# Kernel optimization log

Hardware: AMD Instinct MI355X
Metric: run time of the kernel (lower is better)

## Reference

```python
import jax, jax.numpy as jnp
import numpy as np

B, N, M, NUM_CLASSES = 16, 2048, 2048, 40


def setup_inputs() -> dict:
    key = jax.random.key(0)
    k1, k2, k3, k4 = jax.random.split(key, 4)
    reg = jax.random.normal(k1, (B, N, 3), dtype=jnp.float32)
    point1 = jax.random.normal(k2, (B, M, 3), dtype=jnp.float32)
    # pred is expected to be log-probabilities (output of log_softmax)
    pred = jax.nn.log_softmax(jax.random.normal(k3, (B, NUM_CLASSES), dtype=jnp.float32), axis=-1)
    target = jax.random.randint(k4, (B,), 0, NUM_CLASSES, dtype=jnp.int64)
    return {"reg": reg, "point1": point1, "pred": pred, "target": target}


def _chamfer(x, y):
    # x: [B, N, 3], y: [B, M, 3]
    x2 = jnp.sum(x * x, axis=-1)                      # [B, N]
    y2 = jnp.sum(y * y, axis=-1)                      # [B, M]
    xy = jnp.einsum('bnd,bmd->bnm', x, y)             # [B, N, M]
    d = x2[:, :, None] + y2[:, None, :] - 2.0 * xy    # [B, N, M]
    dist1 = jnp.min(d, axis=2)                        # [B, N] nearest y for each x
    dist2 = jnp.min(d, axis=1)                        # [B, M] nearest x for each y
    return dist1, dist2


def reference(reg, point1, pred, target):
    # NLL loss with mean reduction: -mean(pred[b, target[b]])
    nll = -jnp.mean(jnp.take_along_axis(pred, target[:, None].astype(jnp.int32), axis=1))
    dist1, dist2 = _chamfer(reg, point1)
    reg_loss = jnp.mean(jnp.mean(dist1, axis=1) + jnp.mean(dist2, axis=1))
    return nll + reg_loss
```

## Files before the change

kernel.cpp:

```cpp
#include <hip/hip_runtime.h>
#include <hip/hip_bf16.h>


#define NPTS 2048
#define BATCH 16
#define NCLS 40
#define QB   128
#define KQ   8
#define NSEG 32
#define SEGLEN (NPTS / NSEG)
#define THREADS (QB / KQ * NSEG)

__global__ __launch_bounds__(64) void nll_init_kernel(const float* __restrict__ pred,
                                                      const int* __restrict__ target,
                                                      float* __restrict__ out) {
    int lane = threadIdx.x;
    float v = 0.f;
    if (lane < BATCH) v = pred[lane * NCLS + target[lane]];
    for (int off = 32; off > 0; off >>= 1) v += __shfl_down(v, off);
    if (lane == 0) out[0] = -v * (1.0f / BATCH);
}

__global__ __launch_bounds__(THREADS, 4) void chamfer_kernel(const float* __restrict__ reg,
                                                             const float* __restrict__ pt,
                                                             float* __restrict__ out) {
    int bid = blockIdx.x;
    int dir = bid >> 8;
    int rem = bid & 255;
    int b = rem >> 4;
    int chunk = rem & 15;
    int qbase = chunk * QB;

    const float* __restrict__ X = dir ? pt : reg;
    const float* __restrict__ Y = dir ? reg : pt;

    __shared__ float4 sy[NPTS];
    __shared__ float4 sq[QB];
    __shared__ float  sm[QB * (NSEG + 1)];
    __shared__ float  wsum[THREADS / 64];

    int tid = threadIdx.x;
    int g = tid & 15;
    int s = tid >> 4;

    const float* Yb = Y + (size_t)b * (NPTS * 3);
    for (int p = tid; p < NPTS; p += THREADS) {
        float y0 = Yb[p * 3], y1 = Yb[p * 3 + 1], y2 = Yb[p * 3 + 2];
        sy[p] = make_float4(y0, y1, y2, fmaf(y0, y0, fmaf(y1, y1, y2 * y2)));
    }
    const float* Xb = X + (size_t)b * (NPTS * 3) + (size_t)qbase * 3;
    if (tid < QB) {
        float x0 = Xb[tid * 3], x1 = Xb[tid * 3 + 1], x2 = Xb[tid * 3 + 2];
        sq[tid] = make_float4(-2.f * x0, -2.f * x1, -2.f * x2,
                              fmaf(x0, x0, fmaf(x1, x1, x2 * x2)));
    }
    __syncthreads();

    float ax[KQ], ay[KQ], az[KQ], x2[KQ], mn[KQ];
#pragma unroll
    for (int i = 0; i < KQ; ++i) {
        float4 q = sq[g * KQ + i];
        ax[i] = q.x; ay[i] = q.y; az[i] = q.z; x2[i] = q.w;
        mn[i] = 3.0e38f;
    }

    const float4* ys = sy + s * SEGLEN;
#pragma unroll 4
    for (int m = 0; m < SEGLEN; ++m) {
        float4 y = ys[m];
#pragma unroll
        for (int i = 0; i < KQ; ++i) {
            float d = fmaf(ax[i], y.x, fmaf(ay[i], y.y, fmaf(az[i], y.z, y.w)));
            mn[i] = fminf(mn[i], d);
        }
    }

#pragma unroll
    for (int i = 0; i < KQ; ++i) {
        sm[(g * KQ + i) * (NSEG + 1) + s] = x2[i] + mn[i];
    }
    __syncthreads();

    float v = 0.f;
    if (tid < QB) {
        float mv = 3.0e38f;
#pragma unroll 8
        for (int s2 = 0; s2 < NSEG; ++s2) mv = fminf(mv, sm[tid * (NSEG + 1) + s2]);
        v = mv;
    }
    for (int off = 32; off > 0; off >>= 1) v += __shfl_down(v, off);
    int lane = tid & 63, wid = tid >> 6;
    if (lane == 0) wsum[wid] = v;
    __syncthreads();
    if (tid == 0) {
        float ssum = 0.f;
#pragma unroll
        for (int w = 0; w < THREADS / 64; ++w) ssum += wsum[w];
        atomicAdd(out, ssum * (1.0f / (BATCH * NPTS)));
    }
}

extern "C" void kernel_launch(void* const* d_in, const int* in_sizes, int n_in,
                              void* d_out, int out_size, void* d_ws, size_t ws_size,
                              hipStream_t stream) {
    const float* reg    = (const float*)d_in[0];
    const float* point1 = (const float*)d_in[1];
    const float* pred   = (const float*)d_in[2];
    const int*   target = (const int*)d_in[3];
    float* out = (float*)d_out;

    nll_init_kernel<<<1, 64, 0, stream>>>(pred, target, out);
    chamfer_kernel<<<512, THREADS, 0, stream>>>(reg, point1, out);
}
```

Baseline: 78.14 us.

## Split Y dimension across blocks with atomicMin and precomputed augmented point tables

A preprocessing kernel writes augmented float4 point tables (coordinates plus squared norm, and -2x queries) to workspace and initialises per-query min buffers. The chamfer kernel now tiles the reference set into 512-point chunks, so there are 2048 blocks with smaller shared memory. Partial minima are merged through atomicMin on the float bit pattern, made valid by clamping distances to non-negative. A third kernel sums the minima. This raises parallelism and occupancy, at the cost of two extra launches, workspace traffic and global atomics.

After: 96.17 us. 23.1% more time.

```diff
diff --git a/kernel.cpp b/kernel.cpp
--- a/kernel.cpp
+++ b/kernel.cpp
@@ -5,69 +5,89 @@
 #define NPTS 2048
 #define BATCH 16
 #define NCLS 40
-#define QB   128
-#define KQ   8
+#define QB 128
+#define KQ 8
+#define MB 512
 #define NSEG 32
-#define SEGLEN (NPTS / NSEG)
-#define THREADS (QB / KQ * NSEG)
+#define SEGLEN (MB / NSEG)
+#define THREADS 512
+#define TABLE 65536
 
-__global__ __launch_bounds__(64) void nll_init_kernel(const float* __restrict__ pred,
-                                                      const int* __restrict__ target,
-                                                      float* __restrict__ out) {
-    int lane = threadIdx.x;
-    float v = 0.f;
-    if (lane < BATCH) v = pred[lane * NCLS + target[lane]];
-    for (int off = 32; off > 0; off >>= 1) v += __shfl_down(v, off);
-    if (lane == 0) out[0] = -v * (1.0f / BATCH);
+__global__ __launch_bounds__(256) void init_kernel(const float* __restrict__ reg,
+                                                   const float* __restrict__ pt,
+                                                   const float* __restrict__ pred,
+                                                   const int* __restrict__ target,
+                                                   float* __restrict__ out,
+                                                   float* __restrict__ ws) {
+    unsigned int t = blockIdx.x * 256 + threadIdx.x;
+    unsigned int* minb = (unsigned int*)ws;
+    float4* augY = (float4*)(ws + TABLE);
+    float4* augQ = augY + TABLE;
+
+    minb[t] = 0x7F7FFFFFu;
+
+    int s = t >> 15;
+    int idx = t & 32767;
+    const float* P = s ? pt : reg;
+    float x0 = P[idx * 3], x1 = P[idx * 3 + 1], x2 = P[idx * 3 + 2];
+    float n2 = fmaf(x0, x0, fmaf(x1, x1, x2 * x2));
+    if (s == 0) {
+        augQ[idx]         = make_float4(-2.f * x0, -2.f * x1, -2.f * x2, n2);
+        augY[32768 + idx] = make_float4(x0, x1, x2, n2);
+    } else {
+        augY[idx]         = make_float4(x0, x1, x2, n2);
+        augQ[32768 + idx] = make_float4(-2.f * x0, -2.f * x1, -2.f * x2, n2);
+    }
+
+    if (blockIdx.x == 0 && threadIdx.x < 64) {
+        int lane = threadIdx.x;
+        float v = 0.f;
+        if (lane < BATCH) v = pred[lane * NCLS + target[lane]];
+        for (int off = 32; off > 0; off >>= 1) v += __shfl_down(v, off);
+        if (lane == 0) out[0] = -v * (1.0f / BATCH);
+    }
 }
 
-__global__ __launch_bounds__(THREADS, 4) void chamfer_kernel(const float* __restrict__ reg,
-                                                             const float* __restrict__ pt,
-                                                             float* __restrict__ out) {
+__global__ __launch_bounds__(THREADS, 8) void chamfer_kernel(float* __restrict__ ws) {
+    unsigned int* minb = (unsigned int*)ws;
+    const float4* augY = (const float4*)(ws + TABLE);
+    const float4* augQ = augY + TABLE;
+
     int bid = blockIdx.x;
-    int dir = bid >> 8;
-    int rem = bid & 255;
-    int b = rem >> 4;
-    int chunk = rem & 15;
-    int qbase = chunk * QB;
+    int dir = bid >> 10;
+    int rem = bid & 1023;
+    int b = rem >> 6;
+    int rem2 = rem & 63;
+    int nch = rem2 >> 2;
+    int mq = rem2 & 3;
 
-    const float* __restrict__ X = dir ? pt : reg;
-    const float* __restrict__ Y = dir ? reg : pt;
+    const float4* Yt = augY + dir * 32768 + b * NPTS + mq * MB;
+    const float4* Qt = augQ + dir * 32768 + b * NPTS + nch * QB;
 
-    __shared__ float4 sy[NPTS];
+    __shared__ float4 sy[MB];
     __shared__ float4 sq[QB];
     __shared__ float  sm[QB * (NSEG + 1)];
-    __shared__ float  wsum[THREADS / 64];
 
     int tid = threadIdx.x;
+    sy[tid] = Yt[tid];
+    if (tid < QB) sq[tid] = Qt[tid];
+    __syncthreads();
+
     int g = tid & 15;
     int s = tid >> 4;
 
-    const float* Yb = Y + (size_t)b * (NPTS * 3);
-    for (int p = tid; p < NPTS; p += THREADS) {
-        float y0 = Yb[p * 3], y1 = Yb[p * 3 + 1], y2 = Yb[p * 3 + 2];
-        sy[p] = make_float4(y0, y1, y2, fmaf(y0, y0, fmaf(y1, y1, y2 * y2)));
-    }
-    const float* Xb = X + (size_t)b * (NPTS * 3) + (size_t)qbase * 3;
-    if (tid < QB) {
-        float x0 = Xb[tid * 3], x1 = Xb[tid * 3 + 1], x2 = Xb[tid * 3 + 2];
-        sq[tid] = make_float4(-2.f * x0, -2.f * x1, -2.f * x2,
-                              fmaf(x0, x0, fmaf(x1, x1, x2 * x2)));
-    }
-    __syncthreads();
-
-    float ax[KQ], ay[KQ], az[KQ], x2[KQ], mn[KQ];
+    float ax[KQ], ay[KQ], az[KQ], mn[KQ];
 #pragma unroll
     for (int i = 0; i < KQ; ++i) {
         float4 q = sq[g * KQ + i];
-        ax[i] = q.x; ay[i] = q.y; az[i] = q.z; x2[i] = q.w;
+        ax[i] = q.x; ay[i] = q.y; az[i] = q.z;
         mn[i] = 3.0e38f;
     }
 
-    const float4* ys = sy + s * SEGLEN;
+    const float4* ysp = sy + s * SEGLEN;
 #pragma unroll 4
     for (int m = 0; m < SEGLEN; ++m) {
-        float4 y = ys[m];
+        float4 y = ysp[m];
 #pragma unroll
         for (int i = 0; i < KQ; ++i) {
             float d = fmaf(ax[i], y.x, fmaf(ay[i], y.y, fmaf(az[i], y.z, y.w)));
@@ -77,26 +97,34 @@
 
 #pragma unroll
     for (int i = 0; i < KQ; ++i) {
-        sm[(g * KQ + i) * (NSEG + 1) + s] = x2[i] + mn[i];
+        int qi = g * KQ + i;
+        sm[qi * (NSEG + 1) + s] = fmaxf(sq[qi].w + mn[i], 0.f);
     }
     __syncthreads();
 
-    float v = 0.f;
     if (tid < QB) {
         float mv = 3.0e38f;
 #pragma unroll 8
         for (int s2 = 0; s2 < NSEG; ++s2) mv = fminf(mv, sm[tid * (NSEG + 1) + s2]);
-        v = mv;
+        atomicMin(&minb[dir * 32768 + b * NPTS + nch * QB + tid], __float_as_uint(mv));
     }
+}
+
+__global__ __launch_bounds__(256) void reduce_kernel(const float* __restrict__ ws,
+                                                     float* __restrict__ out) {
+    const uint4* minb4 = (const uint4*)ws;
+    unsigned int t = blockIdx.x * 256 + threadIdx.x;
+    uint4 u = minb4[t];
+    float v = __uint_as_float(u.x) + __uint_as_float(u.y) +
+              __uint_as_float(u.z) + __uint_as_float(u.w);
     for (int off = 32; off > 0; off >>= 1) v += __shfl_down(v, off);
-    int lane = tid & 63, wid = tid >> 6;
+    __shared__ float wsum[4];
+    int lane = threadIdx.x & 63, wid = threadIdx.x >> 6;
     if (lane == 0) wsum[wid] = v;
     __syncthreads();
-    if (tid == 0) {
-        float ssum = 0.f;
-#pragma unroll
-        for (int w = 0; w < THREADS / 64; ++w) ssum += wsum[w];
-        atomicAdd(out, ssum * (1.0f / (BATCH * NPTS)));
+    if (threadIdx.x == 0) {
+        float s = wsum[0] + wsum[1] + wsum[2] + wsum[3];
+        atomicAdd(out, s * (1.0f / (BATCH * NPTS)));
     }
 }
 
@@ -108,7 +136,9 @@
     const float* pred   = (const float*)d_in[2];
     const int*   target = (const int*)d_in[3];
     float* out = (float*)d_out;
+    float* ws  = (float*)d_ws;
 
-    nll_init_kernel<<<1, 64, 0, stream>>>(pred, target, out);
-    chamfer_kernel<<<512, THREADS, 0, stream>>>(reg, point1, out);
+    init_kernel<<<256, 256, 0, stream>>>(reg, point1, pred, target, out, ws);
+    chamfer_kernel<<<2048, THREADS, 0, stream>>>(ws);
+    reduce_kernel<<<64, 256, 0, stream>>>(ws, out);
 }
```
